# Kernel optimization log

Hardware: AMD Instinct MI355X
Metric: run time of the kernel (lower is better)

The kernel has to match this reference:

```python
import jax, jax.numpy as jnp
import numpy as np

N = 200000
E = 3200000
NHID = 128
NUM_GRAPHS = 512


def setup_inputs() -> dict:
    key = jax.random.key(0)
    k_x, k_ei, k_b, k_n, k_w1, k_w2, k_bl = jax.random.split(key, 7)
    x = jax.random.normal(k_x, (N, NHID), dtype=jnp.float32)
    edge_index = jax.random.randint(k_ei, (2, E), 0, N, dtype=jnp.int32)
    batch = jnp.sort(jax.random.randint(k_b, (N,), 0, NUM_GRAPHS, dtype=jnp.int32))
    noise = jax.random.normal(k_n, (N, NHID), dtype=jnp.float32)
    # Generator params (xavier-ish init)
    h = NHID // 2
    W1 = jax.random.normal(k_w1, (NHID, h), dtype=jnp.float32) * np.float32(1.0 / np.sqrt(NHID))
    b1 = jnp.zeros((h,), dtype=jnp.float32)
    W2 = jax.random.normal(k_w2, (h, NHID), dtype=jnp.float32) * np.float32(1.0 / np.sqrt(h))
    b2 = jnp.zeros((NHID,), dtype=jnp.float32)
    return {"x": x, "edge_index": edge_index, "batch": batch, "noise": noise,
            "W1": W1, "b1": b1, "W2": W2, "b2": b2}


def scatter_mean(src_feats, dst_idx, num_nodes):
    # sum messages per destination node, then divide by in-degree (clamped to 1)
    summed = jax.ops.segment_sum(src_feats, dst_idx, num_segments=num_nodes)
    counts = jax.ops.segment_sum(jnp.ones((src_feats.shape[0],), src_feats.dtype),
                                 dst_idx, num_segments=num_nodes)
    return summed / jnp.maximum(counts, 1.0)[:, None]


def reference(x, edge_index, batch, noise, W1, b1, W2, b2):
    src, dst = edge_index[0], edge_index[1]
    # NeighborPropagate: mean aggregation of x_j = x[src] at dst
    x_neighbor = scatter_mean(x[src], dst, x.shape[0])  # [N, nhid]
    g = x_neighbor + noise
    # Generator MLP: relu(fc2(relu(fc1(g))))
    h = jax.nn.relu(g @ W1 + b1)
    x_gen = jax.nn.relu(h @ W2 + b2)
    return x_gen
```

## Files before the change

kernel.cpp:

```cpp
#include <hip/hip_runtime.h>

#define NHID 128
#define HDIM 64
#define EPB 4096
#define MAXBKT 1024
#define CAP 6144

typedef __attribute__((ext_vector_type(8))) short bf16x8;
typedef __attribute__((ext_vector_type(4))) float f32x4;

__device__ __forceinline__ unsigned short f2bf_rn(float f) {
    union { float f; unsigned u; } c; c.f = f;
    unsigned r = c.u + 0x7fffu + ((c.u >> 16) & 1u);
    return (unsigned short)(r >> 16);
}
__device__ __forceinline__ float bf_lo(unsigned d) {
    union { unsigned u; float f; } c; c.u = d << 16; return c.f;
}
__device__ __forceinline__ float bf_hi(unsigned d) {
    union { unsigned u; float f; } c; c.u = d & 0xFFFF0000u; return c.f;
}

__global__ __launch_bounds__(256) void prep_bf16(const float* __restrict__ x,
                                                 unsigned short* __restrict__ xh,
                                                 long long total8) {
    long long t = (long long)blockIdx.x * blockDim.x + threadIdx.x;
    if (t >= total8) return;
    const float4 a = *(const float4*)(x + t * 8);
    const float4 b = *(const float4*)(x + t * 8 + 4);
    ushort4 p, q;
    p.x = f2bf_rn(a.x); p.y = f2bf_rn(a.y); p.z = f2bf_rn(a.z); p.w = f2bf_rn(a.w);
    q.x = f2bf_rn(b.x); q.y = f2bf_rn(b.y); q.z = f2bf_rn(b.z); q.w = f2bf_rn(b.w);
    *(ushort4*)(xh + t * 8) = p;
    *(ushort4*)(xh + t * 8 + 4) = q;
}

__global__ __launch_bounds__(256) void bucket_scatter(const int* __restrict__ src,
                                                      const int* __restrict__ dst,
                                                      int* __restrict__ bucket_cursor,
                                                      unsigned int* __restrict__ bpack,
                                                      int E, int NBKT) {
    __shared__ int h[MAXBKT];
    int t = threadIdx.x;
    long long base = (long long)blockIdx.x * EPB;
    for (int i = t; i < NBKT; i += 256) h[i] = 0;
    __syncthreads();
    for (int p = 0; p < EPB / 256; ++p) {
        long long e = base + p * 256 + t;
        if (e < E) atomicAdd(&h[((unsigned)dst[e]) >> 8], 1);
    }
    __syncthreads();
    for (int i = t; i < NBKT; i += 256) {
        int c = h[i];
        h[i] = c ? (i * CAP + atomicAdd(&bucket_cursor[i], c)) : 0;
    }
    __syncthreads();
    for (int p = 0; p < EPB / 256; ++p) {
        long long e = base + p * 256 + t;
        if (e < E) {
            int d = dst[e];
            int s = src[e];
            int b = ((unsigned)d) >> 8;
            int pos = atomicAdd(&h[b], 1);
            if (pos < (b + 1) * CAP)
                bpack[pos] = (((unsigned)d & 255u) << 24) | (unsigned)s;
        }
    }
}

__global__ __launch_bounds__(256) void bucket_build(unsigned int* __restrict__ bpack,
                                                    const int* __restrict__ bucket_cursor,
                                                    int* __restrict__ cnt,
                                                    int* __restrict__ rowptr,
                                                    int N) {
    __shared__ unsigned ebuf[CAP];
    __shared__ int lc[256];
    __shared__ int sc[256];
    int b = blockIdx.x, t = threadIdx.x;
    int beg = b * CAP;
    int m = bucket_cursor[b]; if (m > CAP) m = CAP;
    lc[t] = 0;
    __syncthreads();
    for (int i = t; i < m; i += 256) {
        unsigned v = bpack[beg + i];
        ebuf[i] = v;
        atomicAdd(&lc[v >> 24], 1);
    }
    __syncthreads();
    int myc = lc[t];
    sc[t] = myc; __syncthreads();
    for (int off = 1; off < 256; off <<= 1) {
        int v = (t >= off) ? sc[t - off] : 0;
        __syncthreads();
        sc[t] += v;
        __syncthreads();
    }
    int excl = sc[t] - myc;
    int node = b * 256 + t;
    if (node < N) { cnt[node] = myc; rowptr[node] = beg + excl; }
    lc[t] = excl;
    __syncthreads();
    for (int i = t; i < m; i += 256) {
        unsigned v = ebuf[i];
        int pos = atomicAdd(&lc[v >> 24], 1);
        bpack[beg + pos] = v & 0xFFFFFFu;
    }
}

__global__ __launch_bounds__(256) void gather_fuse(
    const unsigned short* __restrict__ xh, const unsigned int* __restrict__ perm,
    const int* __restrict__ rowptr, const int* __restrict__ cnt,
    const float* __restrict__ noise, unsigned short* __restrict__ g, int N)
{
    long long t = (long long)blockIdx.x * blockDim.x + threadIdx.x;
    int n = (int)(t >> 4);
    int c = (int)(t & 15);
    if (n >= N) return;
    int beg = rowptr[n];
    int deg = cnt[n];
    float a0 = 0.f, a1 = 0.f, a2 = 0.f, a3 = 0.f, a4 = 0.f, a5 = 0.f, a6 = 0.f, a7 = 0.f;
    const unsigned short* xb = xh + c * 8;
    int i = 0;
    for (; i + 3 < deg; i += 4) {
        unsigned s0 = perm[beg + i];
        unsigned s1 = perm[beg + i + 1];
        unsigned s2 = perm[beg + i + 2];
        unsigned s3 = perm[beg + i + 3];
        uint4 u0 = *(const uint4*)(xb + (long long)s0 * NHID);
        uint4 u1 = *(const uint4*)(xb + (long long)s1 * NHID);
        uint4 u2 = *(const uint4*)(xb + (long long)s2 * NHID);
        uint4 u3 = *(const uint4*)(xb + (long long)s3 * NHID);
        a0 += (bf_lo(u0.x) + bf_lo(u1.x)) + (bf_lo(u2.x) + bf_lo(u3.x));
        a1 += (bf_hi(u0.x) + bf_hi(u1.x)) + (bf_hi(u2.x) + bf_hi(u3.x));
        a2 += (bf_lo(u0.y) + bf_lo(u1.y)) + (bf_lo(u2.y) + bf_lo(u3.y));
        a3 += (bf_hi(u0.y) + bf_hi(u1.y)) + (bf_hi(u2.y) + bf_hi(u3.y));
        a4 += (bf_lo(u0.z) + bf_lo(u1.z)) + (bf_lo(u2.z) + bf_lo(u3.z));
        a5 += (bf_hi(u0.z) + bf_hi(u1.z)) + (bf_hi(u2.z) + bf_hi(u3.z));
        a6 += (bf_lo(u0.w) + bf_lo(u1.w)) + (bf_lo(u2.w) + bf_lo(u3.w));
        a7 += (bf_hi(u0.w) + bf_hi(u1.w)) + (bf_hi(u2.w) + bf_hi(u3.w));
    }
    for (; i < deg; ++i) {
        unsigned s0 = perm[beg + i];
        uint4 u = *(const uint4*)(xb + (long long)s0 * NHID);
        a0 += bf_lo(u.x); a1 += bf_hi(u.x);
        a2 += bf_lo(u.y); a3 += bf_hi(u.y);
        a4 += bf_lo(u.z); a5 += bf_hi(u.z);
        a6 += bf_lo(u.w); a7 += bf_hi(u.w);
    }
    float inv = 1.0f / fmaxf((float)deg, 1.0f);
    const float* nr = noise + (long long)n * NHID + c * 8;
    float4 n0 = *(const float4*)nr;
    float4 n1 = *(const float4*)(nr + 4);
    ushort4 p, q;
    p.x = f2bf_rn(fmaf(a0, inv, n0.x));
    p.y = f2bf_rn(fmaf(a1, inv, n0.y));
    p.z = f2bf_rn(fmaf(a2, inv, n0.z));
    p.w = f2bf_rn(fmaf(a3, inv, n0.w));
    q.x = f2bf_rn(fmaf(a4, inv, n1.x));
    q.y = f2bf_rn(fmaf(a5, inv, n1.y));
    q.z = f2bf_rn(fmaf(a6, inv, n1.z));
    q.w = f2bf_rn(fmaf(a7, inv, n1.w));
    unsigned short* go = g + (long long)n * 256 + c * 8;
    *(ushort4*)go = p;
    *(ushort4*)(go + 4) = q;
}

__global__ __launch_bounds__(256) void mlp_mfma(
    float* out,
    const float* __restrict__ W1, const float* __restrict__ b1,
    const float* __restrict__ W2, const float* __restrict__ b2,
    int N)
{
    __shared__ __align__(16) unsigned short w1t[64 * 136];
    __shared__ __align__(16) unsigned short w2t[128 * 72];
    __shared__ __align__(16) unsigned short ht[4][16 * 72];
    __shared__ float b1s[HDIM];
    __shared__ float b2s[NHID];

    int t = threadIdx.x;
    int wave = t >> 6;
    int lane = t & 63;
    int m = lane & 15;
    int quad = lane >> 4;

    #pragma unroll 4
    for (int p = 0; p < 32; ++p) {
        int idx = p * 256 + t;
        int k = idx >> 6, n = idx & 63;
        w1t[n * 136 + k] = f2bf_rn(W1[idx]);
    }
    #pragma unroll 4
    for (int p = 0; p < 32; ++p) {
        int idx = p * 256 + t;
        int k = idx >> 7, n = idx & 127;
        w2t[n * 72 + k] = f2bf_rn(W2[idx]);
    }
    if (t < HDIM) b1s[t] = b1[t];
    else if (t < HDIM + NHID) b2s[t - HDIM] = b2[t - HDIM];
    __syncthreads();

    int node = blockIdx.x * 64 + wave * 16 + m;
    int nodec = node < N ? node : N - 1;

    const unsigned short* grow = (const unsigned short*)out + (long long)nodec * 256;
    bf16x8 afrag[4];
    #pragma unroll
    for (int kc = 0; kc < 4; ++kc)
        afrag[kc] = *(const bf16x8*)(grow + kc * 32 + quad * 8);

    unsigned short* hw = &ht[wave][0];
    #pragma unroll
    for (int nt = 0; nt < 4; ++nt) {
        f32x4 acc = {0.f, 0.f, 0.f, 0.f};
        #pragma unroll
        for (int kc = 0; kc < 4; ++kc) {
            bf16x8 bfrag = *(const bf16x8*)&w1t[(nt * 16 + m) * 136 + kc * 32 + quad * 8];
            acc = __builtin_amdgcn_mfma_f32_16x16x32_bf16(afrag[kc], bfrag, acc, 0, 0, 0);
        }
        float bb = b1s[nt * 16 + m];
        #pragma unroll
        for (int r = 0; r < 4; ++r) {
            hw[(quad * 4 + r) * 72 + nt * 16 + m] = f2bf_rn(fmaxf(acc[r] + bb, 0.0f));
        }
    }

    bf16x8 a2[2];
    #pragma unroll
    for (int kc = 0; kc < 2; ++kc)
        a2[kc] = *(const bf16x8*)&hw[m * 72 + kc * 32 + quad * 8];

    float* obase = out + ((long long)blockIdx.x * 64 + wave * 16) * NHID;
    #pragma unroll
    for (int nt = 0; nt < 8; ++nt) {
        f32x4 acc = {0.f, 0.f, 0.f, 0.f};
        #pragma unroll
        for (int kc = 0; kc < 2; ++kc) {
            bf16x8 bfrag = *(const bf16x8*)&w2t[(nt * 16 + m) * 72 + kc * 32 + quad * 8];
            acc = __builtin_amdgcn_mfma_f32_16x16x32_bf16(a2[kc], bfrag, acc, 0, 0, 0);
        }
        float bb = b2s[nt * 16 + m];
        #pragma unroll
        for (int r = 0; r < 4; ++r) {
            int orow = blockIdx.x * 64 + wave * 16 + quad * 4 + r;
            if (orow < N)
                obase[(quad * 4 + r) * NHID + nt * 16 + m] = fmaxf(acc[r] + bb, 0.0f);
        }
    }
}

extern "C" void kernel_launch(void* const* d_in, const int* in_sizes, int n_in,
                              void* d_out, int out_size, void* d_ws, size_t ws_size,
                              hipStream_t stream) {
    const float* x     = (const float*)d_in[0];
    const int*   ei    = (const int*)d_in[1];
    const float* noise = (const float*)d_in[3];
    const float* W1    = (const float*)d_in[4];
    const float* b1    = (const float*)d_in[5];
    const float* W2    = (const float*)d_in[6];
    const float* b2    = (const float*)d_in[7];
    float* out = (float*)d_out;

    const int N = in_sizes[2];
    const int E = in_sizes[1] / 2;
    const int* src = ei;
    const int* dst = ei + E;
    const int NBKT = (N + 255) >> 8;

    int* bucket_cursor = (int*)d_ws;
    int* cnt           = bucket_cursor + MAXBKT;
    int* rowptr        = cnt + N;
    unsigned int* bpack = (unsigned int*)(rowptr + N);
    unsigned short* xh  = (unsigned short*)(bpack + (size_t)NBKT * CAP);

    hipMemsetAsync(bucket_cursor, 0, (size_t)MAXBKT * sizeof(int), stream);

    {
        long long total8 = (long long)N * NHID / 8;
        prep_bf16<<<(int)((total8 + 255) / 256), 256, 0, stream>>>(x, xh, total8);
    }
    {
        const int EB = (int)(((long long)E + EPB - 1) / EPB);
        bucket_scatter<<<EB, 256, 0, stream>>>(src, dst, bucket_cursor, bpack, E, NBKT);
    }
    bucket_build<<<NBKT, 256, 0, stream>>>(bpack, bucket_cursor, cnt, rowptr, N);
    {
        long long total = (long long)N * 16;
        gather_fuse<<<(int)((total + 255) / 256), 256, 0, stream>>>(
            xh, bpack, rowptr, cnt, noise, (unsigned short*)out, N);
    }
    mlp_mfma<<<(N + 63) / 64, 256, 0, stream>>>(out, W1, b1, W2, b2, N);
}
```

Before: 501.7 us.

## Replace bucketed CSR build with global-atomic histogram, scan, and placement

```diff
diff --git a/kernel.cpp b/kernel.cpp
--- a/kernel.cpp
+++ b/kernel.cpp
@@ -2,9 +2,6 @@
 
 #define NHID 128
 #define HDIM 64
-#define EPB 4096
-#define MAXBKT 1024
-#define CAP 6144
 
 typedef __attribute__((ext_vector_type(8))) short bf16x8;
 typedef __attribute__((ext_vector_type(4))) float f32x4;
@@ -35,89 +32,71 @@
     *(ushort4*)(xh + t * 8 + 4) = q;
 }
 
-__global__ __launch_bounds__(256) void bucket_scatter(const int* __restrict__ src,
-                                                      const int* __restrict__ dst,
-                                                      int* __restrict__ bucket_cursor,
-                                                      unsigned int* __restrict__ bpack,
-                                                      int E, int NBKT) {
-    __shared__ int h[MAXBKT];
+__global__ __launch_bounds__(256) void hist(const int* __restrict__ dst,
+                                            int* __restrict__ cnt, int E) {
+    int e = blockIdx.x * 256 + threadIdx.x;
+    if (e < E) atomicAdd(&cnt[dst[e]], 1);
+}
+
+__global__ __launch_bounds__(256) void scan_partial(const int* __restrict__ cnt,
+                                                    int* __restrict__ rowptr,
+                                                    int* __restrict__ bsum, int N) {
+    __shared__ int sc[256];
+    int t = threadIdx.x, b = blockIdx.x;
+    int i = b * 256 + t;
+    int v = (i < N) ? cnt[i] : 0;
+    sc[t] = v;
+    __syncthreads();
+    for (int off = 1; off < 256; off <<= 1) {
+        int u = (t >= off) ? sc[t - off] : 0;
+        __syncthreads();
+        sc[t] += u;
+        __syncthreads();
+    }
+    if (i < N) rowptr[i] = sc[t] - v;
+    if (t == 255) bsum[b] = sc[t];
+}
+
+__global__ __launch_bounds__(1024) void scan_bsum(const int* __restrict__ bsum,
+                                                  int* __restrict__ bsumx, int NB) {
+    __shared__ int sc[1024];
     int t = threadIdx.x;
-    long long base = (long long)blockIdx.x * EPB;
-    for (int i = t; i < NBKT; i += 256) h[i] = 0;
+    int v = (t < NB) ? bsum[t] : 0;
+    sc[t] = v;
     __syncthreads();
-    for (int p = 0; p < EPB / 256; ++p) {
-        long long e = base + p * 256 + t;
-        if (e < E) atomicAdd(&h[((unsigned)dst[e]) >> 8], 1);
-    }
-    __syncthreads();
-    for (int i = t; i < NBKT; i += 256) {
-        int c = h[i];
-        h[i] = c ? (i * CAP + atomicAdd(&bucket_cursor[i], c)) : 0;
-    }
-    __syncthreads();
-    for (int p = 0; p < EPB / 256; ++p) {
-        long long e = base + p * 256 + t;
-        if (e < E) {
-            int d = dst[e];
-            int s = src[e];
-            int b = ((unsigned)d) >> 8;
-            int pos = atomicAdd(&h[b], 1);
-            if (pos < (b + 1) * CAP)
-                bpack[pos] = (((unsigned)d & 255u) << 24) | (unsigned)s;
-        }
-    }
-}
-
-__global__ __launch_bounds__(256) void bucket_build(unsigned int* __restrict__ bpack,
-                                                    const int* __restrict__ bucket_cursor,
-                                                    int* __restrict__ cnt,
-                                                    int* __restrict__ rowptr,
-                                                    int N) {
-    __shared__ unsigned ebuf[CAP];
-    __shared__ int lc[256];
-    __shared__ int sc[256];
-    int b = blockIdx.x, t = threadIdx.x;
-    int beg = b * CAP;
-    int m = bucket_cursor[b]; if (m > CAP) m = CAP;
-    lc[t] = 0;
-    __syncthreads();
-    for (int i = t; i < m; i += 256) {
-        unsigned v = bpack[beg + i];
-        ebuf[i] = v;
-        atomicAdd(&lc[v >> 24], 1);
-    }
-    __syncthreads();
-    int myc = lc[t];
-    sc[t] = myc; __syncthreads();
-    for (int off = 1; off < 256; off <<= 1) {
-        int v = (t >= off) ? sc[t - off] : 0;
-        __syncthreads();
-        sc[t] += v;
-        __syncthreads();
-    }
-    int excl = sc[t] - myc;
-    int node = b * 256 + t;
-    if (node < N) { cnt[node] = myc; rowptr[node] = beg + excl; }
-    lc[t] = excl;
-    __syncthreads();
-    for (int i = t; i < m; i += 256) {
-        unsigned v = ebuf[i];
-        int pos = atomicAdd(&lc[v >> 24], 1);
-        bpack[beg + pos] = v & 0xFFFFFFu;
-    }
+    for (int off = 1; off < 1024; off <<= 1) {
+        int u = (t >= off) ? sc[t - off] : 0;
+        __syncthreads();
+        sc[t] += u;
+        __syncthreads();
+    }
+    if (t < NB) bsumx[t] = sc[t] - v;
+}
+
+__global__ __launch_bounds__(256) void place(const int* __restrict__ src,
+                                             const int* __restrict__ dst,
+                                             int* __restrict__ rowptr,
+                                             const int* __restrict__ bsumx,
+                                             unsigned int* __restrict__ perm, int E) {
+    int e = blockIdx.x * 256 + threadIdx.x;
+    if (e >= E) return;
+    int d = dst[e];
+    int old = atomicAdd(&rowptr[d], 1);
+    perm[old + bsumx[((unsigned)d) >> 8]] = (unsigned)src[e];
 }
 
 __global__ __launch_bounds__(256) void gather_fuse(
     const unsigned short* __restrict__ xh, const unsigned int* __restrict__ perm,
     const int* __restrict__ rowptr, const int* __restrict__ cnt,
+    const int* __restrict__ bsumx,
     const float* __restrict__ noise, unsigned short* __restrict__ g, int N)
 {
     long long t = (long long)blockIdx.x * blockDim.x + threadIdx.x;
     int n = (int)(t >> 4);
     int c = (int)(t & 15);
     if (n >= N) return;
-    int beg = rowptr[n];
     int deg = cnt[n];
+    int beg = rowptr[n] + bsumx[((unsigned)n) >> 8] - deg;
     float a0 = 0.f, a1 = 0.f, a2 = 0.f, a3 = 0.f, a4 = 0.f, a5 = 0.f, a6 = 0.f, a7 = 0.f;
     const unsigned short* xb = xh + c * 8;
     int i = 0;
@@ -264,29 +243,29 @@
     const int E = in_sizes[1] / 2;
     const int* src = ei;
     const int* dst = ei + E;
-    const int NBKT = (N + 255) >> 8;
-
-    int* bucket_cursor = (int*)d_ws;
-    int* cnt           = bucket_cursor + MAXBKT;
-    int* rowptr        = cnt + N;
-    unsigned int* bpack = (unsigned int*)(rowptr + N);
-    unsigned short* xh  = (unsigned short*)(bpack + (size_t)NBKT * CAP);
-
-    hipMemsetAsync(bucket_cursor, 0, (size_t)MAXBKT * sizeof(int), stream);
+    const int NB = (N + 255) >> 8;
+
+    int* cnt            = (int*)d_ws;
+    int* rowptr         = cnt + N;
+    int* bsum           = rowptr + N;
+    int* bsumx          = bsum + 1024;
+    unsigned int* perm  = (unsigned int*)(bsumx + 1024);
+    unsigned short* xh  = (unsigned short*)(perm + E);
+
+    hipMemsetAsync(cnt, 0, (size_t)N * sizeof(int), stream);
 
     {
         long long total8 = (long long)N * NHID / 8;
         prep_bf16<<<(int)((total8 + 255) / 256), 256, 0, stream>>>(x, xh, total8);
     }
-    {
-        const int EB = (int)(((long long)E + EPB - 1) / EPB);
-        bucket_scatter<<<EB, 256, 0, stream>>>(src, dst, bucket_cursor, bpack, E, NBKT);
-    }
-    bucket_build<<<NBKT, 256, 0, stream>>>(bpack, bucket_cursor, cnt, rowptr, N);
+    hist<<<(E + 255) / 256, 256, 0, stream>>>(dst, cnt, E);
+    scan_partial<<<NB, 256, 0, stream>>>(cnt, rowptr, bsum, N);
+    scan_bsum<<<1, 1024, 0, stream>>>(bsum, bsumx, NB);
+    place<<<(E + 255) / 256, 256, 0, stream>>>(src, dst, rowptr, bsumx, perm, E);
     {
         long long total = (long long)N * 16;
         gather_fuse<<<(int)((total + 255) / 256), 256, 0, stream>>>(
-            xh, bpack, rowptr, cnt, noise, (unsigned short*)out, N);
+            xh, perm, rowptr, cnt, bsumx, noise, (unsigned short*)out, N);
     }
     mlp_mfma<<<(N + 63) / 64, 256, 0, stream>>>(out, W1, b1, W2, b2, N);
 }
```

Measured after the change: 728.2 us. +45.1%, slower.
